# Performance work log

Hardware: AMD Instinct MI355X
Metric: run time of the kernel (lower is better)

Reference implementation:

```python
import jax, jax.numpy as jnp
import numpy as np

N_QUBITS = 10
Q_DEPTH = 6
MAX_LAYERS = 15
DIM = 2 ** N_QUBITS


def _apply_1q(s, U, w):
    # s: (B, 2^n) real statevector (circuit uses only H/RY/CNOT, all real).
    # Wire 0 is the most-significant bit (PennyLane convention).
    a, b = 2 ** w, 2 ** (N_QUBITS - 1 - w)
    s = s.reshape(-1, a, 2, b)
    if U.ndim == 2:  # gate shared across batch
        s = jnp.einsum('ij,Bajb->Baib', U, s)
    else:            # per-sample gate, U: (B,2,2)
        s = jnp.einsum('Bij,Bajb->Baib', U, s)
    return s.reshape(-1, DIM)


def _apply_cnot(s, c, t):
    # CNOT, control c < target t
    s = s.reshape(-1, 2 ** c, 2, 2 ** (t - c - 1), 2, 2 ** (N_QUBITS - 1 - t))
    s = jnp.stack([s[:, :, 0], jnp.flip(s[:, :, 1], axis=3)], axis=2)
    return s.reshape(-1, DIM)


def _ry(theta):
    # RY(theta) = [[cos t/2, -sin t/2], [sin t/2, cos t/2]]; theta scalar or (B,)
    c, si = jnp.cos(theta / 2.0), jnp.sin(theta / 2.0)
    return jnp.stack([jnp.stack([c, -si], -1), jnp.stack([si, c], -1)], -2)


def _quantum_net(q_in, q_params):
    # q_in: (B, n_qubits) rotation angles; q_params: (max_layers*n_qubits,)
    B = q_in.shape[0]
    qw = q_params.reshape(MAX_LAYERS, N_QUBITS)
    s = jnp.zeros((B, DIM), q_in.dtype).at[:, 0].set(1.0)  # |0...0>
    H = jnp.array([[1.0, 1.0], [1.0, -1.0]], q_in.dtype) / jnp.sqrt(jnp.asarray(2.0, q_in.dtype))
    for w in range(N_QUBITS):
        s = _apply_1q(s, H, w)
    for w in range(N_QUBITS):
        s = _apply_1q(s, _ry(q_in[:, w]), w)
    for k in range(Q_DEPTH):
        for i in range(0, N_QUBITS - 1, 2):
            s = _apply_cnot(s, i, i + 1)
        for i in range(1, N_QUBITS - 1, 2):
            s = _apply_cnot(s, i, i + 1)
        for w in range(N_QUBITS):
            s = _apply_1q(s, _ry(qw[k + 1, w]), w)
    probs = s * s
    # <Z_w> = P(bit_w = 0) - P(bit_w = 1)
    z = []
    for w in range(N_QUBITS):
        p = probs.reshape(-1, 2 ** w, 2, 2 ** (N_QUBITS - 1 - w)).sum(axis=(1, 3))
        z.append(p[:, 0] - p[:, 1])
    return jnp.stack(z, axis=1)  # (B, n_qubits)


def setup_inputs() -> dict:
    key = jax.random.key(0)
    ks = jax.random.split(key, 6)
    B, F, NQ, NC = 8192, 512, N_QUBITS, 2
    q_delta = 0.01
    return {
        'input_features': jax.random.normal(ks[0], (B, F), jnp.float32),
        'W_pre': jax.random.normal(ks[1], (NQ, F), jnp.float32) / np.sqrt(F),
        'b_pre': jnp.zeros((NQ,), jnp.float32),
        'q_params': q_delta * jax.random.normal(ks[2], (MAX_LAYERS * NQ,), jnp.float32),
        'W_post': jax.random.normal(ks[3], (NC, NQ), jnp.float32) / np.sqrt(NQ),
        'b_post': jnp.zeros((NC,), jnp.float32),
    }


def reference(input_features, W_pre, b_pre, q_params, W_post, b_post):
    pre_out = input_features @ W_pre.T + b_pre          # (B, n_qubits)
    q_in = jnp.tanh(pre_out) * (np.pi / 2.0)            # scale to [-pi/2, pi/2]
    q_out = _quantum_net(q_in, q_params)                # (B, n_qubits) PauliZ expvals
    return q_out @ W_post.T + b_post                    # (B, n_classes)
```

## Files before the change

kernel.cpp:

```cpp
#include <hip/hip_runtime.h>
#include <math.h>


#define NQ   10
#define NREG 16
#define DIM  1024

typedef _Float16 f16;
typedef _Float16 f16x8 __attribute__((ext_vector_type(8)));
typedef float    f32x4 __attribute__((ext_vector_type(4)));

template<int BB>
__device__ __forceinline__ void ry_lane(float (&s)[NREG], int lane, float c, float si) {
    float sgn = ((lane >> BB) & 1) ? si : -si;
    #pragma unroll
    for (int r = 0; r < NREG; ++r) {
        float o = __shfl_xor(s[r], 1 << BB);
        s[r] = fmaf(sgn, o, c * s[r]);
    }
}
template<int P>
__device__ __forceinline__ void ry_reg(float (&s)[NREG], float c, float si) {
    const int m = 1 << P;
    #pragma unroll
    for (int r = 0; r < NREG; ++r) {
        if ((r & m) == 0) {
            float a = s[r], b = s[r + m];
            s[r]     = fmaf(c, a, -si * b);
            s[r + m] = fmaf(si, a,  c * b);
        }
    }
}
__device__ __forceinline__ void cnot_5_6(float (&s)[NREG], int lane) {
    bool sel = (lane & 1) != 0;
    #pragma unroll
    for (int r = 0; r < 8; ++r) {
        float a = s[r], b = s[r + 8];
        s[r]     = sel ? b : a;
        s[r + 8] = sel ? a : b;
    }
}
template<int PC, int PT>
__device__ __forceinline__ void cnot_reg(float (&s)[NREG]) {
    #pragma unroll
    for (int r = 0; r < NREG; ++r) {
        if (((r >> PC) & 1) && !((r >> PT) & 1)) {
            float t = s[r];
            s[r] = s[r ^ (1 << PT)];
            s[r ^ (1 << PT)] = t;
        }
    }
}
__device__ __forceinline__ void perm_even(float (&s)[NREG], int lane) {
    int src = lane ^ (((((lane >> 5) & 1) << 4)) | ((((lane >> 3) & 1) << 2)) | (((lane >> 1) & 1)));
    #pragma unroll
    for (int r = 0; r < NREG; ++r) s[r] = __shfl(s[r], src);
}
__device__ __forceinline__ void perm_odd(float (&s)[NREG], int lane) {
    int src = lane ^ (((((lane >> 4) & 1) << 3)) | ((((lane >> 2) & 1) << 1)));
    #pragma unroll
    for (int r = 0; r < NREG; ++r) s[r] = __shfl(s[r], src);
}

#define APPLY_RY_ALL(CARR, SARR, BASE)                                        \
    { float c_, s_;                                                           \
      c_=__shfl(CARR,(BASE)+0); s_=__shfl(SARR,(BASE)+0); ry_lane<5>(s,lane,c_,s_); \
      c_=__shfl(CARR,(BASE)+1); s_=__shfl(SARR,(BASE)+1); ry_lane<4>(s,lane,c_,s_); \
      c_=__shfl(CARR,(BASE)+2); s_=__shfl(SARR,(BASE)+2); ry_lane<3>(s,lane,c_,s_); \
      c_=__shfl(CARR,(BASE)+3); s_=__shfl(SARR,(BASE)+3); ry_lane<2>(s,lane,c_,s_); \
      c_=__shfl(CARR,(BASE)+4); s_=__shfl(SARR,(BASE)+4); ry_lane<1>(s,lane,c_,s_); \
      c_=__shfl(CARR,(BASE)+5); s_=__shfl(SARR,(BASE)+5); ry_lane<0>(s,lane,c_,s_); \
      c_=__shfl(CARR,(BASE)+6); s_=__shfl(SARR,(BASE)+6); ry_reg<3>(s,c_,s_);       \
      c_=__shfl(CARR,(BASE)+7); s_=__shfl(SARR,(BASE)+7); ry_reg<2>(s,c_,s_);       \
      c_=__shfl(CARR,(BASE)+8); s_=__shfl(SARR,(BASE)+8); ry_reg<1>(s,c_,s_);       \
      c_=__shfl(CARR,(BASE)+9); s_=__shfl(SARR,(BASE)+9); ry_reg<0>(s,c_,s_); }

__device__ __forceinline__ void async16(const void* g, void* l) {
    __builtin_amdgcn_global_load_lds(
        (const __attribute__((address_space(1))) void*)g,
        (__attribute__((address_space(3))) void*)l, 16, 0, 0);
}

#define BARRIER() do { __builtin_amdgcn_s_barrier(); __builtin_amdgcn_sched_barrier(0); } while (0)
#define VMCNT12() asm volatile("s_waitcnt vmcnt(12)" ::: "memory")
#define VMCNT6()  asm volatile("s_waitcnt vmcnt(6)" ::: "memory")
#define VMCNT0()  asm volatile("s_waitcnt vmcnt(0)" ::: "memory")

__global__ __launch_bounds__(256) void ka_prepare(
    const float* __restrict__ X, const float* __restrict__ Wpre,
    const float* __restrict__ bpre, const float* __restrict__ qp,
    f16* __restrict__ psi0, f16* __restrict__ Arm, float* __restrict__ z, int B)
{
    const int tid = threadIdx.x, lane = tid & 63, wv = tid >> 6;

    {
        int idx = blockIdx.x * 256 + tid;
        if (idx < 8192 * NQ) z[idx] = 0.0f;
    }

    {
        int sample = blockIdx.x * 4 + wv;
        if (sample < B) {
            const float* xrow = X + (size_t)sample * 512;
            float4 x0 = ((const float4*)xrow)[lane];
            float4 x1 = ((const float4*)xrow)[64 + lane];
            float acc[NQ];
            #pragma unroll
            for (int q = 0; q < NQ; ++q) {
                const float* wr = Wpre + q * 512;
                float4 w0 = ((const float4*)wr)[lane];
                float4 w1 = ((const float4*)wr)[64 + lane];
                float a = x0.x * w0.x;
                a = fmaf(x0.y, w0.y, a); a = fmaf(x0.z, w0.z, a); a = fmaf(x0.w, w0.w, a);
                a = fmaf(x1.x, w1.x, a); a = fmaf(x1.y, w1.y, a);
                a = fmaf(x1.z, w1.z, a); a = fmaf(x1.w, w1.w, a);
                acc[q] = a;
            }
            #pragma unroll
            for (int q = 0; q < NQ; ++q) {
                float v = acc[q];
                #pragma unroll
                for (int d = 32; d >= 1; d >>= 1) v += __shfl_xor(v, d);
                acc[q] = v;
            }
            float pre = acc[0];
            #pragma unroll
            for (int q = 1; q < NQ; ++q) pre = (lane == q) ? acc[q] : pre;
            float c45 = 0.0f, s45 = 0.0f;
            if (lane < NQ) {
                float th = tanhf(pre + bpre[lane]) * 1.5707963267948966f;
                sincosf(0.5f * th + 0.7853981633974483f, &s45, &c45);
            }
            float lv = 1.0f;
            #pragma unroll
            for (int w = 0; w < 6; ++w) {
                float f0 = __shfl(c45, w), f1 = __shfl(s45, w);
                lv *= ((lane >> (5 - w)) & 1) ? f1 : f0;
            }
            float c6 = __shfl(c45, 6), s6 = __shfl(s45, 6);
            float c7 = __shfl(c45, 7), s7 = __shfl(s45, 7);
            float c8 = __shfl(c45, 8), s8 = __shfl(s45, 8);
            float c9 = __shfl(c45, 9), s9 = __shfl(s45, 9);
            float g01[4] = {c6 * c7, c6 * s7, s6 * c7, s6 * s7};
            float g23[4] = {c8 * c9, c8 * s9, s8 * c9, s8 * s9};
            union { f16 h[16]; float4 v[2]; } u;
            #pragma unroll
            for (int r = 0; r < NREG; ++r)
                u.h[r] = (f16)(lv * g01[r >> 2] * g23[r & 3]);
            float4* dst = (float4*)((char*)psi0 + (size_t)sample * 2048 + lane * 32);
            dst[0] = u.v[0];
            dst[1] = u.v[1];
        }
    }

    if (wv < 2) {
        int row = blockIdx.x * 2 + wv;
        if (row < DIM) {
            float cw = 1.0f, swn = 0.0f;
            if (lane < 60) {
                float s_, c_;
                sincosf(0.5f * qp[10 + lane], &s_, &c_);
                cw = c_; swn = -s_;
            }
            float s[NREG];
            int srcLane = row >> 4, srcReg = row & 15;
            #pragma unroll
            for (int r = 0; r < NREG; ++r)
                s[r] = (lane == srcLane && r == srcReg) ? 1.0f : 0.0f;
            for (int kk = 6; kk >= 1; --kk) {
                APPLY_RY_ALL(cw, swn, (kk - 1) * 10);
                perm_odd(s, lane);
                cnot_5_6(s, lane);
                cnot_reg<2, 1>(s);
                perm_even(s, lane);
                cnot_reg<3, 2>(s);
                cnot_reg<1, 0>(s);
            }
            union { f16 h[16]; float4 v[2]; } u;
            #pragma unroll
            for (int r = 0; r < NREG; ++r) u.h[r] = (f16)s[r];
            float4* dst = (float4*)((char*)Arm + (size_t)row * 2048 + lane * 32);
            dst[0] = u.v[0];
            dst[1] = u.v[1];
        }
    }
}

__global__ __launch_bounds__(512) void kb_gemm_measure(
    const f16* __restrict__ psi0, const f16* __restrict__ Arm,
    float* __restrict__ z)
{
    __shared__ __align__(16) char smem[147456];
    const int tid = threadIdx.x, lane = tid & 63, wv = tid >> 6;
    const int p = blockIdx.x;
    const int mB = (p & 7) + 8 * (p >> 5), nB = (p >> 3) & 3;
    const size_t tM = (size_t)mB * 128, tN = (size_t)nB * 256;
    f16* As_[3] = { (f16*)smem,           (f16*)(smem + 49152), (f16*)(smem + 98304) };
    f16* Bs_[3] = { (f16*)(smem + 16384), (f16*)(smem + 65536), (f16*)(smem + 114688) };
    const int wm = (wv >> 2) * 64, wn = (wv & 3) * 64;

    f32x4 acc[4][4] = {};

    const f16* ga[2]; int ldsoA[2];
    const f16* gb[4]; int ldsoB[4];
    #pragma unroll
    for (int q = 0; q < 2; ++q) {
        int slot = q * 512 + tid;
        int row = slot >> 3, gp = slot & 7, g = gp ^ (row & 7);
        ga[q] = psi0 + (tM + row) * 1024 + g * 8;
        ldsoA[q] = slot * 16;
    }
    #pragma unroll
    for (int q = 0; q < 4; ++q) {
        int slot = q * 512 + tid;
        int row = slot >> 3, gp = slot & 7, g = gp ^ (row & 7);
        gb[q] = Arm + (tN + row) * 1024 + g * 8;
        ldsoB[q] = slot * 16;
    }

    auto stage = [&](f16* Ab, f16* Bb, int kt) {
        #pragma unroll
        for (int q = 0; q < 2; ++q) async16(ga[q] + kt, (char*)Ab + ldsoA[q]);
        #pragma unroll
        for (int q = 0; q < 4; ++q) async16(gb[q] + kt, (char*)Bb + ldsoB[q]);
    };
    auto compute = [&](const f16* Ab, const f16* Bb) {
        #pragma unroll
        for (int ks = 0; ks < 2; ++ks) {
            f16x8 af[4], bf[4];
            const int gpb = ks * 4 + (lane >> 4);
            const int gpx = gpb ^ (lane & 7);
            #pragma unroll
            for (int i = 0; i < 4; ++i) {
                int rowA = wm + i * 16 + (lane & 15);
                af[i] = *(const f16x8*)(Ab + rowA * 64 + gpx * 8);
            }
            #pragma unroll
            for (int j = 0; j < 4; ++j) {
                int rowB = wn + j * 16 + (lane & 15);
                bf[j] = *(const f16x8*)(Bb + rowB * 64 + gpx * 8);
            }
            #pragma unroll
            for (int i = 0; i < 4; ++i)
                #pragma unroll
                for (int j = 0; j < 4; ++j)
                    acc[i][j] = __builtin_amdgcn_mfma_f32_16x16x32_f16(af[i], bf[j], acc[i][j], 0, 0, 0);
        }
    };

    f16 *Ac = As_[0], *Bc = Bs_[0];
    f16 *An = As_[1], *Bn = Bs_[1];
    f16 *Af = As_[2], *Bf = Bs_[2];
    stage(Ac, Bc, 0);
    stage(An, Bn, 64);
    #pragma unroll 1
    for (int t = 0; t < 14; ++t) {
        stage(Af, Bf, (t + 2) * 64);
        VMCNT12();
        BARRIER();
        compute(Ac, Bc);
        BARRIER();
        f16* ta = Ac; f16* tb = Bc;
        Ac = An; Bc = Bn; An = Af; Bn = Bf; Af = ta; Bf = tb;
    }
    VMCNT6();  BARRIER(); compute(Ac, Bc); BARRIER();
    VMCNT0();  BARRIER(); compute(An, Bn);

    __syncthreads();
    float* zbuf = (float*)smem;
    float* zb = zbuf + (wv & 3) * 1280;
    const float sg0 = (nB & 2)        ? -1.0f : 1.0f;
    const float sg1 = (nB & 1)        ? -1.0f : 1.0f;
    const float sg2 = ((wv >> 1) & 1) ? -1.0f : 1.0f;
    const float sg3 = (wv & 1)        ? -1.0f : 1.0f;

    #pragma unroll
    for (int i = 0; i < 4; ++i) {
        #pragma unroll
        for (int t = 0; t < 4; ++t) {
            float p0 = acc[i][0][t] * acc[i][0][t];
            float p1 = acc[i][1][t] * acc[i][1][t];
            float p2 = acc[i][2][t] * acc[i][2][t];
            float p3 = acc[i][3][t] * acc[i][3][t];
            float t0  = (p0 + p1) + (p2 + p3);
            float tw5 = (p0 - p1) + (p2 - p3);
            float tw4 = (p0 + p1) - (p2 + p3);
            float s1 = __shfl_xor(t0, 1);
            float Av = t0 + s1;
            float Bv = (lane & 1) ? s1 - t0 : t0 - s1;
            float sA = __shfl_xor(Av, 2), sB = __shfl_xor(Bv, 2);
            float AP = Av + sA;
            float AM = (lane & 2) ? sA - Av : Av - sA;
            float BP = Bv + sB;
            float sAP = __shfl_xor(AP, 4), sAM = __shfl_xor(AM, 4), sBP = __shfl_xor(BP, 4);
            float APP = AP + sAP;
            float APM = (lane & 4) ? sAP - AP : AP - sAP;
            float AMP = AM + sAM;
            float BPP = BP + sBP;
            float a1 = __shfl_xor(APP, 8), a2 = __shfl_xor(APM, 8);
            float a3 = __shfl_xor(AMP, 8), a4 = __shfl_xor(BPP, 8);
            float T0 = APP + a1;
            float S6 = (lane & 8) ? a1 - APP : APP - a1;
            float S7 = APM + a2;
            float S8 = AMP + a3;
            float S9 = BPP + a4;
            float T5 = tw5, T4 = tw4;
            T5 += __shfl_xor(T5, 1); T5 += __shfl_xor(T5, 2);
            T5 += __shfl_xor(T5, 4); T5 += __shfl_xor(T5, 8);
            T4 += __shfl_xor(T4, 1); T4 += __shfl_xor(T4, 2);
            T4 += __shfl_xor(T4, 4); T4 += __shfl_xor(T4, 8);
            if ((lane & 15) == 0) {
                int row = wm + i * 16 + (lane >> 4) * 4 + t;
                float* d = zb + row * 10;
                d[0] = sg0 * T0; d[1] = sg1 * T0; d[2] = sg2 * T0; d[3] = sg3 * T0;
                d[4] = T4; d[5] = T5;
                d[6] = S6; d[7] = S7; d[8] = S8; d[9] = S9;
            }
        }
    }
    __syncthreads();
    for (int idx = tid; idx < 1280; idx += 512) {
        float v = (zbuf[idx] + zbuf[1280 + idx]) + (zbuf[2560 + idx] + zbuf[3840 + idx]);
        int row = idx / 10, w = idx - row * 10;
        atomicAdd(&z[((size_t)tM + row) * 10 + w], v);
    }
}

__global__ __launch_bounds__(256) void kc_post(
    const float* __restrict__ z, const float* __restrict__ Wpost,
    const float* __restrict__ bpost, float* __restrict__ out, int B)
{
    int gid = blockIdx.x * 256 + threadIdx.x;
    if (gid >= B) return;
    const float* zp = z + (size_t)gid * NQ;
    float o0 = bpost[0], o1 = bpost[1];
    #pragma unroll
    for (int w = 0; w < NQ; ++w) {
        float zw = zp[w];
        o0 = fmaf(zw, Wpost[w], o0);
        o1 = fmaf(zw, Wpost[NQ + w], o1);
    }
    out[(size_t)gid * 2 + 0] = o0;
    out[(size_t)gid * 2 + 1] = o1;
}

template<int BC, int BT>
__device__ __forceinline__ void cnot_lane(float (&s)[NREG], int lane) {
    int src = ((lane >> BC) & 1) ? (lane ^ (1 << BT)) : lane;
    #pragma unroll
    for (int r = 0; r < NREG; ++r) s[r] = __shfl(s[r], src);
}

__global__ __launch_bounds__(256) void hybrid_head_fallback(
    const float* __restrict__ X, const float* __restrict__ Wpre,
    const float* __restrict__ bpre, const float* __restrict__ qp,
    const float* __restrict__ Wpost, const float* __restrict__ bpost,
    float* __restrict__ out, int B)
{
    const int lane = threadIdx.x & 63;
    const int wave = threadIdx.x >> 6;
    const int sample = blockIdx.x * 4 + wave;
    if (sample >= B) return;

    const float* xrow = X + (size_t)sample * 512;
    float4 x0 = ((const float4*)xrow)[lane];
    float4 x1 = ((const float4*)xrow)[64 + lane];
    float acc[NQ];
    #pragma unroll
    for (int q = 0; q < NQ; ++q) {
        const float* wr = Wpre + q * 512;
        float4 w0 = ((const float4*)wr)[lane];
        float4 w1 = ((const float4*)wr)[64 + lane];
        float a = x0.x * w0.x;
        a = fmaf(x0.y, w0.y, a); a = fmaf(x0.z, w0.z, a); a = fmaf(x0.w, w0.w, a);
        a = fmaf(x1.x, w1.x, a); a = fmaf(x1.y, w1.y, a);
        a = fmaf(x1.z, w1.z, a); a = fmaf(x1.w, w1.w, a);
        acc[q] = a;
    }
    #pragma unroll
    for (int q = 0; q < NQ; ++q) {
        float v = acc[q];
        #pragma unroll
        for (int d = 32; d >= 1; d >>= 1) v += __shfl_xor(v, d);
        acc[q] = v;
    }
    float pre = acc[0];
    #pragma unroll
    for (int q = 1; q < NQ; ++q) pre = (lane == q) ? acc[q] : pre;
    float cth = 1.0f, sth = 0.0f;
    if (lane < NQ) {
        float th = tanhf(pre + bpre[lane]) * 1.5707963267948966f;
        sincosf(0.5f * th, &sth, &cth);
    }
    float cw = 1.0f, sw = 0.0f;
    if (lane < 60) sincosf(0.5f * qp[10 + lane], &sw, &cw);

    float s[NREG];
    #pragma unroll
    for (int r = 0; r < NREG; ++r) s[r] = 0.03125f;
    APPLY_RY_ALL(cth, sth, 0);
    for (int k = 0; k < 6; ++k) {
        perm_even(s, lane);
        cnot_reg<3, 2>(s);
        cnot_reg<1, 0>(s);
        perm_odd(s, lane);
        cnot_5_6(s, lane);
        cnot_reg<2, 1>(s);
        APPLY_RY_ALL(cw, sw, k * 10);
    }
    float p[NREG], tot = 0.0f;
    #pragma unroll
    for (int r = 0; r < NREG; ++r) { p[r] = s[r] * s[r]; tot += p[r]; }
    float z[NQ];
    #pragma unroll
    for (int w = 0; w < 6; ++w) z[w] = ((lane >> (5 - w)) & 1) ? -tot : tot;
    z[6] = z[7] = z[8] = z[9] = 0.0f;
    #pragma unroll
    for (int r = 0; r < NREG; ++r) {
        z[6] += ((r >> 3) & 1) ? -p[r] : p[r];
        z[7] += ((r >> 2) & 1) ? -p[r] : p[r];
        z[8] += ((r >> 1) & 1) ? -p[r] : p[r];
        z[9] += ((r >> 0) & 1) ? -p[r] : p[r];
    }
    #pragma unroll
    for (int w = 0; w < NQ; ++w) {
        float v = z[w];
        #pragma unroll
        for (int d = 32; d >= 1; d >>= 1) v += __shfl_xor(v, d);
        z[w] = v;
    }
    if (lane < 2) {
        const float* wp = Wpost + lane * NQ;
        float o = bpost[lane];
        #pragma unroll
        for (int w = 0; w < NQ; ++w) o = fmaf(z[w], wp[w], o);
        out[(size_t)sample * 2 + lane] = o;
    }
}

extern "C" void kernel_launch(void* const* d_in, const int* in_sizes, int n_in,
                              void* d_out, int out_size, void* d_ws, size_t ws_size,
                              hipStream_t stream) {
    const float* X     = (const float*)d_in[0];
    const float* Wpre  = (const float*)d_in[1];
    const float* bpre  = (const float*)d_in[2];
    const float* qp    = (const float*)d_in[3];
    const float* Wpost = (const float*)d_in[4];
    const float* bpost = (const float*)d_in[5];
    float* out = (float*)d_out;
    int B = in_sizes[0] / 512;

    size_t psi0_b = (size_t)B * DIM * sizeof(f16);
    size_t arm_b  = (size_t)DIM * DIM * sizeof(f16);
    size_t z_b    = (size_t)B * NQ * sizeof(float);
    size_t need = psi0_b + arm_b + z_b;

    if (B != 8192 || ws_size < need) {
        hipLaunchKernelGGL(hybrid_head_fallback, dim3((B + 3) / 4), dim3(256), 0, stream,
                           X, Wpre, bpre, qp, Wpost, bpost, out, B);
        return;
    }

    char* ws = (char*)d_ws;
    f16*   psi0 = (f16*)ws;
    f16*   Arm  = (f16*)(ws + psi0_b);
    float* z    = (float*)(ws + psi0_b + arm_b);

    hipLaunchKernelGGL(ka_prepare, dim3(2048), dim3(256), 0, stream,
                       X, Wpre, bpre, qp, psi0, Arm, z, B);
    hipLaunchKernelGGL(kb_gemm_measure, dim3(256), dim3(512), 0, stream,
                       psi0, Arm, z);
    hipLaunchKernelGGL(kc_post, dim3(32), dim3(256), 0, stream,
                       z, Wpost, bpost, out, B);
}
```

Before: 117.9 us.

## Generate product-state A tiles on the fly instead of materializing psi0

The prepare kernel now writes only 20 per-sample cos/sin factors instead of a full 1024-element fp16 product statevector. The GEMM kernel rebuilds each A tile in registers from these factors and writes it to LDS, so only the B operand (Arm) is streamed with async global-to-LDS loads in a triple buffer, while A is double buffered. This removes a 16 MB write and re-read of psi0 from HBM. In exchange the GEMM does extra ALU work and LDS stores each k-step, and adds lgkmcnt waits to the pipeline.

New measurement: 116.6 us. No clear change (-1.1%).

```diff
diff --git a/kernel.cpp b/kernel.cpp
--- a/kernel.cpp
+++ b/kernel.cpp
@@ -82,14 +82,15 @@
 }
 
 #define BARRIER() do { __builtin_amdgcn_s_barrier(); __builtin_amdgcn_sched_barrier(0); } while (0)
-#define VMCNT12() asm volatile("s_waitcnt vmcnt(12)" ::: "memory")
-#define VMCNT6()  asm volatile("s_waitcnt vmcnt(6)" ::: "memory")
+#define VMCNT8()  asm volatile("s_waitcnt vmcnt(8)" ::: "memory")
+#define VMCNT4()  asm volatile("s_waitcnt vmcnt(4)" ::: "memory")
 #define VMCNT0()  asm volatile("s_waitcnt vmcnt(0)" ::: "memory")
+#define LGKMCNT0() asm volatile("s_waitcnt lgkmcnt(0)" ::: "memory")
 
 __global__ __launch_bounds__(256) void ka_prepare(
     const float* __restrict__ X, const float* __restrict__ Wpre,
     const float* __restrict__ bpre, const float* __restrict__ qp,
-    f16* __restrict__ psi0, f16* __restrict__ Arm, float* __restrict__ z, int B)
+    float* __restrict__ fac, f16* __restrict__ Arm, float* __restrict__ z, int B)
 {
     const int tid = threadIdx.x, lane = tid & 63, wv = tid >> 6;
 
@@ -126,30 +127,14 @@
             float pre = acc[0];
             #pragma unroll
             for (int q = 1; q < NQ; ++q) pre = (lane == q) ? acc[q] : pre;
-            float c45 = 0.0f, s45 = 0.0f;
             if (lane < NQ) {
                 float th = tanhf(pre + bpre[lane]) * 1.5707963267948966f;
+                float s45, c45;
                 sincosf(0.5f * th + 0.7853981633974483f, &s45, &c45);
-            }
-            float lv = 1.0f;
-            #pragma unroll
-            for (int w = 0; w < 6; ++w) {
-                float f0 = __shfl(c45, w), f1 = __shfl(s45, w);
-                lv *= ((lane >> (5 - w)) & 1) ? f1 : f0;
-            }
-            float c6 = __shfl(c45, 6), s6 = __shfl(s45, 6);
-            float c7 = __shfl(c45, 7), s7 = __shfl(s45, 7);
-            float c8 = __shfl(c45, 8), s8 = __shfl(s45, 8);
-            float c9 = __shfl(c45, 9), s9 = __shfl(s45, 9);
-            float g01[4] = {c6 * c7, c6 * s7, s6 * c7, s6 * s7};
-            float g23[4] = {c8 * c9, c8 * s9, s8 * c9, s8 * s9};
-            union { f16 h[16]; float4 v[2]; } u;
-            #pragma unroll
-            for (int r = 0; r < NREG; ++r)
-                u.h[r] = (f16)(lv * g01[r >> 2] * g23[r & 3]);
-            float4* dst = (float4*)((char*)psi0 + (size_t)sample * 2048 + lane * 32);
-            dst[0] = u.v[0];
-            dst[1] = u.v[1];
+                float* fp = fac + (size_t)sample * 20;
+                fp[2 * lane]     = c45;
+                fp[2 * lane + 1] = s45;
+            }
         }
     }
 
@@ -187,29 +172,24 @@
 }
 
 __global__ __launch_bounds__(512) void kb_gemm_measure(
-    const f16* __restrict__ psi0, const f16* __restrict__ Arm,
+    const float* __restrict__ fac, const f16* __restrict__ Arm,
     float* __restrict__ z)
 {
-    __shared__ __align__(16) char smem[147456];
+    __shared__ __align__(16) char smem[131072];
     const int tid = threadIdx.x, lane = tid & 63, wv = tid >> 6;
     const int p = blockIdx.x;
     const int mB = (p & 7) + 8 * (p >> 5), nB = (p >> 3) & 3;
     const size_t tM = (size_t)mB * 128, tN = (size_t)nB * 256;
-    f16* As_[3] = { (f16*)smem,           (f16*)(smem + 49152), (f16*)(smem + 98304) };
-    f16* Bs_[3] = { (f16*)(smem + 16384), (f16*)(smem + 65536), (f16*)(smem + 114688) };
+    f16* A0 = (f16*)smem;
+    f16* A1 = (f16*)(smem + 16384);
+    f16* B0 = (f16*)(smem + 32768);
+    f16* B1 = (f16*)(smem + 65536);
+    f16* B2 = (f16*)(smem + 98304);
     const int wm = (wv >> 2) * 64, wn = (wv & 3) * 64;
 
     f32x4 acc[4][4] = {};
 
-    const f16* ga[2]; int ldsoA[2];
     const f16* gb[4]; int ldsoB[4];
-    #pragma unroll
-    for (int q = 0; q < 2; ++q) {
-        int slot = q * 512 + tid;
-        int row = slot >> 3, gp = slot & 7, g = gp ^ (row & 7);
-        ga[q] = psi0 + (tM + row) * 1024 + g * 8;
-        ldsoA[q] = slot * 16;
-    }
     #pragma unroll
     for (int q = 0; q < 4; ++q) {
         int slot = q * 512 + tid;
@@ -217,13 +197,49 @@
         gb[q] = Arm + (tN + row) * 1024 + g * 8;
         ldsoB[q] = slot * 16;
     }
-
-    auto stage = [&](f16* Ab, f16* Bb, int kt) {
-        #pragma unroll
-        for (int q = 0; q < 2; ++q) async16(ga[q] + kt, (char*)Ab + ldsoA[q]);
-        #pragma unroll
-        for (int q = 0; q < 4; ++q) async16(gb[q] + kt, (char*)Bb + ldsoB[q]);
+    auto stageB = [&](f16* Bb, int t) {
+        #pragma unroll
+        for (int q = 0; q < 4; ++q) async16(gb[q] + t * 64, (char*)Bb + ldsoB[q]);
     };
+
+    float c0[2], s0[2], c1[2], s1[2], c2[2], s2[2], c3[2], s3[2];
+    float pgl[2][8];
+    int ldsoA[2];
+    #pragma unroll
+    for (int q = 0; q < 2; ++q) {
+        int slot = q * 512 + tid;
+        int row = slot >> 3, gp = slot & 7, g = gp ^ (row & 7);
+        ldsoA[q] = slot * 16;
+        const float* fp = fac + (tM + row) * 20;
+        float4 f01 = ((const float4*)fp)[0];
+        float4 f23 = ((const float4*)fp)[1];
+        float4 f45 = ((const float4*)fp)[2];
+        float4 f67 = ((const float4*)fp)[3];
+        float4 f89 = ((const float4*)fp)[4];
+        c0[q] = f01.x; s0[q] = f01.y; c1[q] = f01.z; s1[q] = f01.w;
+        c2[q] = f23.x; s2[q] = f23.y; c3[q] = f23.z; s3[q] = f23.w;
+        float pm = (((g >> 2) & 1) ? f45.y : f45.x)
+                 * (((g >> 1) & 1) ? f45.w : f45.z)
+                 * ((g & 1)        ? f67.y : f67.x);
+        #pragma unroll
+        for (int e = 0; e < 8; ++e) {
+            pgl[q][e] = pm * (((e >> 2) & 1) ? f67.w : f67.z)
+                           * (((e >> 1) & 1) ? f89.y : f89.x)
+                           * ((e & 1)        ? f89.w : f89.z);
+        }
+    }
+    auto writeA = [&](f16* Ab, int t) {
+        #pragma unroll
+        for (int q = 0; q < 2; ++q) {
+            float ph = ((t & 8) ? s0[q] : c0[q]) * ((t & 4) ? s1[q] : c1[q])
+                     * ((t & 2) ? s2[q] : c2[q]) * ((t & 1) ? s3[q] : c3[q]);
+            f16x8 v;
+            #pragma unroll
+            for (int e = 0; e < 8; ++e) v[e] = (f16)(ph * pgl[q][e]);
+            *(f16x8*)((char*)Ab + ldsoA[q]) = v;
+        }
+    };
+
     auto compute = [&](const f16* Ab, const f16* Bb) {
         #pragma unroll
         for (int ks = 0; ks < 2; ++ks) {
@@ -248,23 +264,27 @@
         }
     };
 
-    f16 *Ac = As_[0], *Bc = Bs_[0];
-    f16 *An = As_[1], *Bn = Bs_[1];
-    f16 *Af = As_[2], *Bf = Bs_[2];
-    stage(Ac, Bc, 0);
-    stage(An, Bn, 64);
+    f16 *Bc = B0, *Bn = B1, *Bf = B2;
+    stageB(Bc, 0);
+    stageB(Bn, 1);
     #pragma unroll 1
     for (int t = 0; t < 14; ++t) {
-        stage(Af, Bf, (t + 2) * 64);
-        VMCNT12();
+        stageB(Bf, t + 2);
+        writeA((t & 1) ? A1 : A0, t);
+        VMCNT8();
+        LGKMCNT0();
         BARRIER();
-        compute(Ac, Bc);
+        compute((t & 1) ? A1 : A0, Bc);
         BARRIER();
-        f16* ta = Ac; f16* tb = Bc;
-        Ac = An; Bc = Bn; An = Af; Bn = Bf; Af = ta; Bf = tb;
-    }
-    VMCNT6();  BARRIER(); compute(Ac, Bc); BARRIER();
-    VMCNT0();  BARRIER(); compute(An, Bn);
+        f16* tmp = Bc; Bc = Bn; Bn = Bf; Bf = tmp;
+    }
+    writeA(A0, 14);
+    VMCNT4(); LGKMCNT0(); BARRIER();
+    compute(A0, Bc);
+    BARRIER();
+    writeA(A1, 15);
+    VMCNT0(); LGKMCNT0(); BARRIER();
+    compute(A1, Bn);
 
     __syncthreads();
     float* zbuf = (float*)smem;
@@ -285,9 +305,9 @@
             float t0  = (p0 + p1) + (p2 + p3);
             float tw5 = (p0 - p1) + (p2 - p3);
             float tw4 = (p0 + p1) - (p2 + p3);
-            float s1 = __shfl_xor(t0, 1);
-            float Av = t0 + s1;
-            float Bv = (lane & 1) ? s1 - t0 : t0 - s1;
+            float s1_ = __shfl_xor(t0, 1);
+            float Av = t0 + s1_;
+            float Bv = (lane & 1) ? s1_ - t0 : t0 - s1_;
             float sA = __shfl_xor(Av, 2), sB = __shfl_xor(Bv, 2);
             float AP = Av + sA;
             float AM = (lane & 2) ? sA - Av : Av - sA;
@@ -450,10 +470,10 @@
     float* out = (float*)d_out;
     int B = in_sizes[0] / 512;
 
-    size_t psi0_b = (size_t)B * DIM * sizeof(f16);
+    size_t fac_b  = (size_t)B * 20 * sizeof(float);
     size_t arm_b  = (size_t)DIM * DIM * sizeof(f16);
     size_t z_b    = (size_t)B * NQ * sizeof(float);
-    size_t need = psi0_b + arm_b + z_b;
+    size_t need = fac_b + arm_b + z_b;
 
     if (B != 8192 || ws_size < need) {
         hipLaunchKernelGGL(hybrid_head_fallback, dim3((B + 3) / 4), dim3(256), 0, stream,
@@ -462,14 +482,14 @@
     }
 
     char* ws = (char*)d_ws;
-    f16*   psi0 = (f16*)ws;
-    f16*   Arm  = (f16*)(ws + psi0_b);
-    float* z    = (float*)(ws + psi0_b + arm_b);
+    float* fac = (float*)ws;
+    f16*   Arm = (f16*)(ws + fac_b);
+    float* z   = (float*)(ws + fac_b + arm_b);
 
     hipLaunchKernelGGL(ka_prepare, dim3(2048), dim3(256), 0, stream,
-                       X, Wpre, bpre, qp, psi0, Arm, z, B);
+                       X, Wpre, bpre, qp, fac, Arm, z, B);
     hipLaunchKernelGGL(kb_gemm_measure, dim3(256), dim3(512), 0, stream,
-                       psi0, Arm, z);
+                       fac, Arm, z);
     hipLaunchKernelGGL(kc_post, dim3(32), dim3(256), 0, stream,
                        z, Wpost, bpost, out, B);
 }
```
